# Kernel tuning notes

Measured on AMD Instinct MI355X. Metric: run time of the kernel, lower is better.

## Reference

```python
import jax, jax.numpy as jnp
import numpy as np

N_NODES = 50000
N_EDGES = 1200000
IN_CH = 128
HID = 64
HEADS = 1
OUT_CH = 64
NEG_SLOPE = 0.2


def setup_inputs() -> dict:
    key = jax.random.key(0)
    ks = jax.random.split(key, 9)
    x = jax.random.normal(ks[0], (N_NODES, IN_CH), dtype=jnp.float32)
    edge_index = jax.random.randint(ks[1], (2, N_EDGES), 0, N_NODES, dtype=jnp.int64)
    edge_weight = jax.random.uniform(ks[2], (N_EDGES,), dtype=jnp.float32)
    # GATv2Conv params: separate lin_l / lin_r (share_weights=False), attention vector, bias
    s_in = 1.0 / np.sqrt(IN_CH)
    W_l = jax.random.uniform(ks[3], (HEADS * HID, IN_CH), minval=-s_in, maxval=s_in, dtype=jnp.float32)
    W_r = jax.random.uniform(ks[4], (HEADS * HID, IN_CH), minval=-s_in, maxval=s_in, dtype=jnp.float32)
    att = jax.random.normal(ks[5], (HEADS, HID), dtype=jnp.float32) * (1.0 / np.sqrt(HID))
    bias_conv = jnp.zeros((HEADS * HID,), dtype=jnp.float32)
    s_h = 1.0 / np.sqrt(HEADS * HID)
    W_lin = jax.random.uniform(ks[6], (OUT_CH, HEADS * HID), minval=-s_h, maxval=s_h, dtype=jnp.float32)
    b_lin = jax.random.uniform(ks[7], (OUT_CH,), minval=-s_h, maxval=s_h, dtype=jnp.float32)
    return {"x": x, "edge_index": edge_index, "edge_weight": edge_weight,
            "W_l": W_l, "W_r": W_r, "att": att, "bias_conv": bias_conv,
            "W_lin": W_lin, "b_lin": b_lin}


def reference(x, edge_index, edge_weight, W_l, W_r, att, bias_conv, W_lin, b_lin):
    N = x.shape[0]
    H, C = att.shape
    # add self loops (GATv2Conv default add_self_loops=True)
    loop = jnp.arange(N, dtype=edge_index.dtype)
    src = jnp.concatenate([edge_index[0], loop])  # [E+N] source j
    dst = jnp.concatenate([edge_index[1], loop])  # [E+N] target i
    # linear projections -> [N, H, C]
    xl = (x @ W_l.T).reshape(N, H, C)
    xr = (x @ W_r.T).reshape(N, H, C)
    # per-edge GATv2 logits: att . LeakyReLU(xl_j + xr_i)
    e = jax.nn.leaky_relu(xl[src] + xr[dst], NEG_SLOPE)       # [E, H, C]
    logits = jnp.einsum('ehc,hc->eh', e, att)                 # [E, H]
    # segment softmax over incoming edges of each target node
    m = jax.ops.segment_max(logits, dst, num_segments=N)       # [N, H]
    m = jnp.where(jnp.isfinite(m), m, 0.0)
    expv = jnp.exp(logits - m[dst])                            # [E, H]
    denom = jax.ops.segment_sum(expv, dst, num_segments=N)     # [N, H]
    alpha = expv / (denom[dst] + 1e-16)                        # [E, H]
    # dropout(p=0.2) on alpha: identity in eval mode
    # scatter-weighted aggregation of source features
    msg = alpha[:, :, None] * xl[src]                          # [E, H, C]
    out = jax.ops.segment_sum(msg, dst, num_segments=N)        # [N, H, C]
    out = out.reshape(N, H * C) + bias_conv
    out = jax.nn.elu(out)
    return out @ W_lin.T + b_lin
```

## Files before the change

kernel.cpp:

```cpp
#include <hip/hip_runtime.h>

#define IN_CH 128
#define HID 64
#define NEG 0.2f

typedef short bf16x8 __attribute__((ext_vector_type(8)));
typedef float f32x4  __attribute__((ext_vector_type(4)));

__device__ __forceinline__ unsigned short f2bf(float f) {
    unsigned u = __float_as_uint(f);
    u += 0x7fffu + ((u >> 16) & 1u);
    return (unsigned short)(u >> 16);
}
__device__ __forceinline__ float bf2f(unsigned short h) {
    return __uint_as_float((unsigned)h << 16);
}

__global__ __launch_bounds__(512, 4) void proj_kernel(
    const float* __restrict__ x, const float* __restrict__ W_l,
    const float* __restrict__ W_r,
    unsigned short* __restrict__ xlb, float* __restrict__ xr,
    const int* __restrict__ dst, int* __restrict__ bcnt,
    int nN, int E)
{
    __shared__ unsigned short A_hi[64 * 136];
    __shared__ unsigned short A_lo[64 * 136];
    int tid = threadIdx.x;
    int nb = blockIdx.x * 64;
    int lane = tid & 63;
    int wid = __builtin_amdgcn_readfirstlane(tid >> 6);
    int mat = wid >> 2;
    int ct  = (wid & 3) * 16;
    int n = lane & 15, quad = lane >> 4;

    const float* __restrict__ W = mat ? W_r : W_l;
    bf16x8 Bh[4], Bl[4];
    #pragma unroll
    for (int s = 0; s < 4; ++s) {
        const float* wr = W + (size_t)(ct + n) * IN_CH + s * 32 + quad * 8;
        float4 w0 = *(const float4*)(wr);
        float4 w1 = *(const float4*)(wr + 4);
        float wf[8] = {w0.x, w0.y, w0.z, w0.w, w1.x, w1.y, w1.z, w1.w};
        #pragma unroll
        for (int j = 0; j < 8; ++j) {
            unsigned short h = f2bf(wf[j]);
            Bh[s][j] = (short)h;
            Bl[s][j] = (short)f2bf(wf[j] - bf2f(h));
        }
    }

    #pragma unroll
    for (int it = 0; it < 2; ++it) {
        int gi = it * 512 + tid;
        int row = gi >> 4, c8 = gi & 15;
        int node = nb + row;
        uint4 hi = make_uint4(0, 0, 0, 0), lo = make_uint4(0, 0, 0, 0);
        if (node < nN) {
            const float* xp = x + (size_t)node * IN_CH + c8 * 8;
            float4 f0 = *(const float4*)(xp);
            float4 f1 = *(const float4*)(xp + 4);
            float xf[8] = {f0.x, f0.y, f0.z, f0.w, f1.x, f1.y, f1.z, f1.w};
            unsigned hh[8], ll[8];
            #pragma unroll
            for (int j = 0; j < 8; ++j) {
                unsigned short h = f2bf(xf[j]);
                hh[j] = h;
                ll[j] = f2bf(xf[j] - bf2f(h));
            }
            hi = make_uint4(hh[0] | (hh[1] << 16), hh[2] | (hh[3] << 16),
                            hh[4] | (hh[5] << 16), hh[6] | (hh[7] << 16));
            lo = make_uint4(ll[0] | (ll[1] << 16), ll[2] | (ll[3] << 16),
                            ll[4] | (ll[5] << 16), ll[6] | (ll[7] << 16));
        }
        *(uint4*)(&A_hi[row * 136 + c8 * 8]) = hi;
        *(uint4*)(&A_lo[row * 136 + c8 * 8]) = lo;
    }
    __syncthreads();

    #pragma unroll
    for (int mt = 0; mt < 4; ++mt) {
        f32x4 d = {0.f, 0.f, 0.f, 0.f};
        int arow = (mt * 16 + n) * 136 + quad * 8;
        #pragma unroll
        for (int s = 0; s < 4; ++s) {
            bf16x8 ah = *(const bf16x8*)(&A_hi[arow + s * 32]);
            bf16x8 al = *(const bf16x8*)(&A_lo[arow + s * 32]);
            d = __builtin_amdgcn_mfma_f32_16x16x32_bf16(ah, Bh[s], d, 0, 0, 0);
            d = __builtin_amdgcn_mfma_f32_16x16x32_bf16(ah, Bl[s], d, 0, 0, 0);
            d = __builtin_amdgcn_mfma_f32_16x16x32_bf16(al, Bh[s], d, 0, 0, 0);
        }
        #pragma unroll
        for (int r = 0; r < 4; ++r) {
            int node = nb + mt * 16 + quad * 4 + r;
            if (node < nN) {
                if (mat)
                    xr[(size_t)node * HID + ct + n] = d[r];
                else
                    xlb[(size_t)node * HID + ct + n] = f2bf(d[r]);
            }
        }
    }

    __syncthreads();
    int* lh = (int*)A_hi;
    #pragma unroll
    for (int i = 0; i < 2; ++i) lh[i * 512 + tid] = 0;
    __syncthreads();
    int E4 = E >> 2;
    int gstride = gridDim.x * 512;
    for (int i = blockIdx.x * 512 + tid; i < E4; i += gstride) {
        int4 v = *(const int4*)(dst + i * 4);
        atomicAdd(&lh[v.x >> 6], 1);
        atomicAdd(&lh[v.y >> 6], 1);
        atomicAdd(&lh[v.z >> 6], 1);
        atomicAdd(&lh[v.w >> 6], 1);
    }
    if (blockIdx.x == 0 && tid == 0) {
        for (int i = E4 * 4; i < E; ++i) atomicAdd(&bcnt[dst[i] >> 6], 1);
    }
    __syncthreads();
    #pragma unroll
    for (int i = 0; i < 2; ++i) {
        int b = i * 512 + tid;
        int c = lh[b];
        if (c) atomicAdd(&bcnt[b], c);
    }
}

__global__ __launch_bounds__(256) void bscan_kernel(
    const int* __restrict__ bcnt, int* __restrict__ bstart,
    int* __restrict__ gcursor)
{
    __shared__ int wsum[4];
    int tid = threadIdx.x, lane = tid & 63, w = tid >> 6;
    int4 v = ((const int4*)bcnt)[tid];
    int e1 = v.x, e2 = v.x + v.y, e3 = e2 + v.z;
    int run = e3 + v.w;
    int sv = run;
    #pragma unroll
    for (int d = 1; d < 64; d <<= 1) {
        int t = __shfl_up(sv, d, 64);
        if (lane >= d) sv += t;
    }
    if (lane == 63) wsum[w] = sv;
    __syncthreads();
    if (tid < 4) {
        int t = wsum[tid];
        #pragma unroll
        for (int d = 1; d < 4; d <<= 1) {
            int u = __shfl_up(t, d, 64);
            if (tid >= d) t += u;
        }
        wsum[tid] = t;
    }
    __syncthreads();
    int off = (w ? wsum[w - 1] : 0) + (sv - run);
    int4 o = make_int4(off, off + e1, off + e2, off + e3);
    ((int4*)(bstart))[tid] = o;
    ((int4*)(gcursor))[tid] = o;
}

__global__ __launch_bounds__(256) void part_kernel(
    const int* __restrict__ src, const int* __restrict__ dst,
    int* __restrict__ gcursor, unsigned* __restrict__ pairs, int E)
{
    __shared__ int lhist[1024];
    __shared__ int lbase[1024];
    __shared__ int lcnt[1024];
    int tid = threadIdx.x;
    #pragma unroll
    for (int i = 0; i < 4; ++i) {
        lhist[i * 256 + tid] = 0;
        lcnt[i * 256 + tid] = 0;
    }
    __syncthreads();
    int base = blockIdx.x * 8192 + tid * 32;
    unsigned wreg[32];
    unsigned short bk[32];
    int v = E - base;
    v = v < 0 ? 0 : (v > 32 ? 32 : v);
    #pragma unroll
    for (int q = 0; q < 8; ++q) {
        int i = base + q * 4;
        if (i + 3 < E) {
            int4 s4 = *(const int4*)(src + i);
            int4 d4 = *(const int4*)(dst + i);
            wreg[q*4+0] = (unsigned)s4.x | (((unsigned)d4.x & 63u) << 16); bk[q*4+0] = d4.x >> 6;
            wreg[q*4+1] = (unsigned)s4.y | (((unsigned)d4.y & 63u) << 16); bk[q*4+1] = d4.y >> 6;
            wreg[q*4+2] = (unsigned)s4.z | (((unsigned)d4.z & 63u) << 16); bk[q*4+2] = d4.z >> 6;
            wreg[q*4+3] = (unsigned)s4.w | (((unsigned)d4.w & 63u) << 16); bk[q*4+3] = d4.w >> 6;
        } else {
            for (int j = 0; j < 4; ++j) {
                int e = i + j;
                if (e < E) {
                    int s = src[e], d = dst[e];
                    wreg[q*4+j] = (unsigned)s | (((unsigned)d & 63u) << 16);
                    bk[q*4+j] = d >> 6;
                }
            }
        }
    }
    for (int q = 0; q < v; ++q) atomicAdd(&lhist[bk[q]], 1);
    __syncthreads();
    #pragma unroll
    for (int i = 0; i < 4; ++i) {
        int b = i * 256 + tid;
        int c = lhist[b];
        lbase[b] = c ? atomicAdd(&gcursor[b], c) : 0;
    }
    __syncthreads();
    for (int q = 0; q < v; ++q) {
        int b = bk[q];
        int r = atomicAdd(&lcnt[b], 1);
        pairs[lbase[b] + r] = wreg[q];
    }
}

__global__ __launch_bounds__(256, 8) void gat_sorted(
    const unsigned short* __restrict__ xlb, const float* __restrict__ xr,
    const unsigned* __restrict__ pairs, const int* __restrict__ bstart,
    const float* __restrict__ att, const float* __restrict__ bias_conv,
    const float* __restrict__ W_lin, const float* __restrict__ b_lin,
    float* __restrict__ out, int nN)
{
    __shared__ unsigned short sorted[2048];
    __shared__ unsigned short Hhi[32 * 72];
    __shared__ unsigned short Hlo[32 * 72];
    __shared__ int cnt[32];
    __shared__ int rs[33];
    __shared__ int cur[32];
    int tid = threadIdx.x;
    if (tid < 32) cnt[tid] = 0;
    __syncthreads();

    int blk = blockIdx.x;
    int b  = blk >> 1;
    int hh = blk & 1;
    int e0 = bstart[b];
    int M = bstart[b + 1] - e0;
    if (M > 2048) M = 2048;

    unsigned ew[8];
    int ne = 0;
    for (int i = tid; i < M; i += 256) {
        unsigned w = pairs[e0 + i];
        int d6 = (w >> 16) & 63;
        if ((d6 >> 5) == hh) {
            ew[ne++] = w;
            atomicAdd(&cnt[d6 & 31], 1);
        }
    }
    __syncthreads();
    if (tid < 32) {
        int c = cnt[tid];
        int s = c;
        #pragma unroll
        for (int d = 1; d < 32; d <<= 1) {
            int t = __shfl_up(s, d, 64);
            if (tid >= d) s += t;
        }
        rs[tid] = s - c;
        cur[tid] = s - c;
        if (tid == 31) rs[32] = s;
    }
    __syncthreads();
    for (int q = 0; q < ne; ++q) {
        unsigned w = ew[q];
        int d = (w >> 16) & 31;
        int p = atomicAdd(&cur[d], 1);
        sorted[p] = (unsigned short)(w & 0xFFFFu);
    }
    __syncthreads();

    int lane = tid & 63, wv = tid >> 6;
    int g = lane >> 4, gl = lane & 15;
    const float4 att4 = *(const float4*)(att + gl * 4);
    int nb = b * 64 + hh * 32;
    for (int t = 0; t < 8; ++t) {
        int nl = wv * 8 + t;
        int node = nb + nl;
        if (node >= nN) break;
        const float4 xr4 = *(const float4*)(xr + (size_t)node * HID + gl * 4);
        float4 acc = make_float4(0.f, 0.f, 0.f, 0.f);
        float denom = 0.f;
        if (g == 0) {
            ushort4 us = *(const ushort4*)(xlb + (size_t)node * HID + gl * 4);
            float xsx = bf2f(us.x), xsy = bf2f(us.y), xsz = bf2f(us.z), xsw = bf2f(us.w);
            float tx = xsx + xr4.x, ty = xsy + xr4.y;
            float tz = xsz + xr4.z, tw = xsw + xr4.w;
            float r =          att4.x * (fmaxf(tx, 0.f) + NEG * fminf(tx, 0.f));
            r = fmaf(att4.y, fmaxf(ty, 0.f) + NEG * fminf(ty, 0.f), r);
            r = fmaf(att4.z, fmaxf(tz, 0.f) + NEG * fminf(tz, 0.f), r);
            r = fmaf(att4.w, fmaxf(tw, 0.f) + NEG * fminf(tw, 0.f), r);
            r += __shfl_xor(r, 1, 64);
            r += __shfl_xor(r, 2, 64);
            r += __shfl_xor(r, 4, 64);
            r += __shfl_xor(r, 8, 64);
            float ev = __expf(r);
            denom = ev;
            acc.x = ev * xsx; acc.y = ev * xsy;
            acc.z = ev * xsz; acc.w = ev * xsw;
        }
        int s0 = rs[nl], s1 = rs[nl + 1];
        int last = s1 - 1;
        for (int base = s0; base < s1; base += 16) {
            int kb = base + g * 4;
            int k0 = (kb     <= last) ? kb     : last;
            int k1 = (kb + 1 <= last) ? kb + 1 : last;
            int k2 = (kb + 2 <= last) ? kb + 2 : last;
            int k3 = (kb + 3 <= last) ? kb + 3 : last;
            int j0 = sorted[k0], j1 = sorted[k1], j2 = sorted[k2], j3 = sorted[k3];
            ushort4 ua = *(const ushort4*)(xlb + (size_t)j0 * HID + gl * 4);
            ushort4 ub = *(const ushort4*)(xlb + (size_t)j1 * HID + gl * 4);
            ushort4 uc = *(const ushort4*)(xlb + (size_t)j2 * HID + gl * 4);
            ushort4 ud = *(const ushort4*)(xlb + (size_t)j3 * HID + gl * 4);
            float xax = bf2f(ua.x), xay = bf2f(ua.y), xaz = bf2f(ua.z), xaw = bf2f(ua.w);
            float xbx = bf2f(ub.x), xby = bf2f(ub.y), xbz = bf2f(ub.z), xbw = bf2f(ub.w);
            float xcx = bf2f(uc.x), xcy = bf2f(uc.y), xcz = bf2f(uc.z), xcw = bf2f(uc.w);
            float xdx = bf2f(ud.x), xdy = bf2f(ud.y), xdz = bf2f(ud.z), xdw = bf2f(ud.w);

            float t0, t1, t2, t3, ra, rb, rc, rd;
            t0 = xax + xr4.x; t1 = xay + xr4.y; t2 = xaz + xr4.z; t3 = xaw + xr4.w;
            ra =          att4.x * (fmaxf(t0, 0.f) + NEG * fminf(t0, 0.f));
            ra = fmaf(att4.y, fmaxf(t1, 0.f) + NEG * fminf(t1, 0.f), ra);
            ra = fmaf(att4.z, fmaxf(t2, 0.f) + NEG * fminf(t2, 0.f), ra);
            ra = fmaf(att4.w, fmaxf(t3, 0.f) + NEG * fminf(t3, 0.f), ra);
            t0 = xbx + xr4.x; t1 = xby + xr4.y; t2 = xbz + xr4.z; t3 = xbw + xr4.w;
            rb =          att4.x * (fmaxf(t0, 0.f) + NEG * fminf(t0, 0.f));
            rb = fmaf(att4.y, fmaxf(t1, 0.f) + NEG * fminf(t1, 0.f), rb);
            rb = fmaf(att4.z, fmaxf(t2, 0.f) + NEG * fminf(t2, 0.f), rb);
            rb = fmaf(att4.w, fmaxf(t3, 0.f) + NEG * fminf(t3, 0.f), rb);
            t0 = xcx + xr4.x; t1 = xcy + xr4.y; t2 = xcz + xr4.z; t3 = xcw + xr4.w;
            rc =          att4.x * (fmaxf(t0, 0.f) + NEG * fminf(t0, 0.f));
            rc = fmaf(att4.y, fmaxf(t1, 0.f) + NEG * fminf(t1, 0.f), rc);
            rc = fmaf(att4.z, fmaxf(t2, 0.f) + NEG * fminf(t2, 0.f), rc);
            rc = fmaf(att4.w, fmaxf(t3, 0.f) + NEG * fminf(t3, 0.f), rc);
            t0 = xdx + xr4.x; t1 = xdy + xr4.y; t2 = xdz + xr4.z; t3 = xdw + xr4.w;
            rd =          att4.x * (fmaxf(t0, 0.f) + NEG * fminf(t0, 0.f));
            rd = fmaf(att4.y, fmaxf(t1, 0.f) + NEG * fminf(t1, 0.f), rd);
            rd = fmaf(att4.z, fmaxf(t2, 0.f) + NEG * fminf(t2, 0.f), rd);
            rd = fmaf(att4.w, fmaxf(t3, 0.f) + NEG * fminf(t3, 0.f), rd);

            ra += __shfl_xor(ra, 1, 64); rb += __shfl_xor(rb, 1, 64);
            rc += __shfl_xor(rc, 1, 64); rd += __shfl_xor(rd, 1, 64);
            ra += __shfl_xor(ra, 2, 64); rb += __shfl_xor(rb, 2, 64);
            rc += __shfl_xor(rc, 2, 64); rd += __shfl_xor(rd, 2, 64);
            ra += __shfl_xor(ra, 4, 64); rb += __shfl_xor(rb, 4, 64);
            rc += __shfl_xor(rc, 4, 64); rd += __shfl_xor(rd, 4, 64);
            ra += __shfl_xor(ra, 8, 64); rb += __shfl_xor(rb, 8, 64);
            rc += __shfl_xor(rc, 8, 64); rd += __shfl_xor(rd, 8, 64);

            float ea = (kb     < s1) ? __expf(ra) : 0.f;
            float eb = (kb + 1 < s1) ? __expf(rb) : 0.f;
            float ec = (kb + 2 < s1) ? __expf(rc) : 0.f;
            float ed = (kb + 3 < s1) ? __expf(rd) : 0.f;
            denom += (ea + eb) + (ec + ed);
            acc.x = fmaf(ea, xax, acc.x); acc.x = fmaf(eb, xbx, acc.x);
            acc.x = fmaf(ec, xcx, acc.x); acc.x = fmaf(ed, xdx, acc.x);
            acc.y = fmaf(ea, xay, acc.y); acc.y = fmaf(eb, xby, acc.y);
            acc.y = fmaf(ec, xcy, acc.y); acc.y = fmaf(ed, xdy, acc.y);
            acc.z = fmaf(ea, xaz, acc.z); acc.z = fmaf(eb, xbz, acc.z);
            acc.z = fmaf(ec, xcz, acc.z); acc.z = fmaf(ed, xdz, acc.z);
            acc.w = fmaf(ea, xaw, acc.w); acc.w = fmaf(eb, xbw, acc.w);
            acc.w = fmaf(ec, xcw, acc.w); acc.w = fmaf(ed, xdw, acc.w);
        }
        denom += __shfl_xor(denom, 16, 64);
        denom += __shfl_xor(denom, 32, 64);
        acc.x += __shfl_xor(acc.x, 16, 64); acc.x += __shfl_xor(acc.x, 32, 64);
        acc.y += __shfl_xor(acc.y, 16, 64); acc.y += __shfl_xor(acc.y, 32, 64);
        acc.z += __shfl_xor(acc.z, 16, 64); acc.z += __shfl_xor(acc.z, 32, 64);
        acc.w += __shfl_xor(acc.w, 16, 64); acc.w += __shfl_xor(acc.w, 32, 64);
        float inv = 1.f / (denom + 1e-16f);
        float4 b4 = *(const float4*)(bias_conv + gl * 4);
        float hx = fmaf(acc.x, inv, b4.x);
        float hy = fmaf(acc.y, inv, b4.y);
        float hz = fmaf(acc.z, inv, b4.z);
        float hw = fmaf(acc.w, inv, b4.w);
        hx = (hx > 0.f) ? hx : (__expf(hx) - 1.f);
        hy = (hy > 0.f) ? hy : (__expf(hy) - 1.f);
        hz = (hz > 0.f) ? hz : (__expf(hz) - 1.f);
        hw = (hw > 0.f) ? hw : (__expf(hw) - 1.f);
        if (g == 0) {
            unsigned short hix = f2bf(hx), hiy = f2bf(hy),
                           hiz = f2bf(hz), hiw = f2bf(hw);
            ushort4 vhi = make_ushort4(hix, hiy, hiz, hiw);
            ushort4 vlo = make_ushort4(f2bf(hx - bf2f(hix)), f2bf(hy - bf2f(hiy)),
                                       f2bf(hz - bf2f(hiz)), f2bf(hw - bf2f(hiw)));
            *(ushort4*)(&Hhi[nl * 72 + gl * 4]) = vhi;
            *(ushort4*)(&Hlo[nl * 72 + gl * 4]) = vlo;
        }
    }
    __syncthreads();

    bf16x8 Wh[2], Wl[2];
    #pragma unroll
    for (int s = 0; s < 2; ++s) {
        const float* wr = W_lin + (size_t)(wv * 16 + gl) * HID + s * 32 + g * 8;
        float4 w0 = *(const float4*)(wr);
        float4 w1 = *(const float4*)(wr + 4);
        float wf[8] = {w0.x, w0.y, w0.z, w0.w, w1.x, w1.y, w1.z, w1.w};
        #pragma unroll
        for (int j = 0; j < 8; ++j) {
            unsigned short h = f2bf(wf[j]);
            Wh[s][j] = (short)h;
            Wl[s][j] = (short)f2bf(wf[j] - bf2f(h));
        }
    }
    float blin = b_lin[wv * 16 + gl];
    #pragma unroll
    for (int mt = 0; mt < 2; ++mt) {
        f32x4 d = {0.f, 0.f, 0.f, 0.f};
        int arow = (mt * 16 + gl) * 72 + g * 8;
        #pragma unroll
        for (int s = 0; s < 2; ++s) {
            bf16x8 ah = *(const bf16x8*)(&Hhi[arow + s * 32]);
            bf16x8 al = *(const bf16x8*)(&Hlo[arow + s * 32]);
            d = __builtin_amdgcn_mfma_f32_16x16x32_bf16(ah, Wh[s], d, 0, 0, 0);
            d = __builtin_amdgcn_mfma_f32_16x16x32_bf16(ah, Wl[s], d, 0, 0, 0);
            d = __builtin_amdgcn_mfma_f32_16x16x32_bf16(al, Wh[s], d, 0, 0, 0);
        }
        #pragma unroll
        for (int r = 0; r < 4; ++r) {
            int node = nb + mt * 16 + g * 4 + r;
            if (node < nN)
                out[(size_t)node * HID + wv * 16 + gl] = d[r] + blin;
        }
    }
}

extern "C" void kernel_launch(void* const* d_in, const int* in_sizes, int n_in,
                              void* d_out, int out_size, void* d_ws, size_t ws_size,
                              hipStream_t stream) {
    const float* x      = (const float*)d_in[0];
    const int*   ei     = (const int*)d_in[1];
    const float* W_l    = (const float*)d_in[3];
    const float* W_r    = (const float*)d_in[4];
    const float* att    = (const float*)d_in[5];
    const float* bias_c = (const float*)d_in[6];
    const float* W_lin  = (const float*)d_in[7];
    const float* b_lin  = (const float*)d_in[8];
    float* out = (float*)d_out;

    int N = in_sizes[0] / IN_CH;
    int E = in_sizes[2];
    const int* srcp = ei;
    const int* dstp = ei + E;
    int NB = (N + 63) / 64;

    char* ws = (char*)d_ws;
    float* xr = (float*)ws;
    unsigned short* xlb = (unsigned short*)(xr + (size_t)N * HID);
    int* bcnt    = (int*)(xlb + (size_t)N * HID);
    int* bstart  = bcnt + 1024;
    int* gcursor = bstart + 1056;
    unsigned* pairs = (unsigned*)(gcursor + 1024);

    hipMemsetAsync(bcnt, 0, 1024 * sizeof(int), stream);
    proj_kernel<<<NB, 512, 0, stream>>>(x, W_l, W_r, xlb, xr, dstp, bcnt, N, E);
    bscan_kernel<<<1, 256, 0, stream>>>(bcnt, bstart, gcursor);
    part_kernel<<<(E + 8191) / 8192, 256, 0, stream>>>(srcp, dstp, gcursor, pairs, E);
    gat_sorted<<<NB * 2, 256, 0, stream>>>(xlb, xr, pairs, bstart,
                                           att, bias_c, W_lin, b_lin, out, N);
}
```

Measured before the change: 200.9 us.

## Merge histogram, scan, and partition into one grid-synced prep kernel

Moves the destination-bucket histogram out of the projection kernel and combines histogram, prefix scan and partition into one persistent kernel. The stages are separated by software grid barriers on atomic counters. Block 0 of the projection kernel now zeroes the counters in place of a separate memset, which removes two launches. The LeakyReLU attention dot is also rewritten as a*t + b*|t| with pre-scaled att vectors, which cuts ALU ops per edge. The spin barriers depend on all 512 blocks being co-resident, and the partition pass now reads src/dst twice.

```diff
diff --git a/kernel.cpp b/kernel.cpp
--- a/kernel.cpp
+++ b/kernel.cpp
@@ -20,8 +20,8 @@
     const float* __restrict__ x, const float* __restrict__ W_l,
     const float* __restrict__ W_r,
     unsigned short* __restrict__ xlb, float* __restrict__ xr,
-    const int* __restrict__ dst, int* __restrict__ bcnt,
-    int nN, int E)
+    int* __restrict__ zbuf,
+    int nN)
 {
     __shared__ unsigned short A_hi[64 * 136];
     __shared__ unsigned short A_lo[64 * 136];
@@ -32,6 +32,10 @@
     int mat = wid >> 2;
     int ct  = (wid & 3) * 16;
     int n = lane & 15, quad = lane >> 4;
+
+    if (blockIdx.x == 0) {
+        for (int i = tid; i < 1056; i += 512) zbuf[i] = 0;
+    }
 
     const float* __restrict__ W = mat ? W_r : W_l;
     bf16x8 Bh[4], Bl[4];
@@ -100,108 +104,95 @@
             }
         }
     }
-
-    __syncthreads();
-    int* lh = (int*)A_hi;
-    #pragma unroll
-    for (int i = 0; i < 2; ++i) lh[i * 512 + tid] = 0;
-    __syncthreads();
-    int E4 = E >> 2;
-    int gstride = gridDim.x * 512;
-    for (int i = blockIdx.x * 512 + tid; i < E4; i += gstride) {
-        int4 v = *(const int4*)(dst + i * 4);
-        atomicAdd(&lh[v.x >> 6], 1);
-        atomicAdd(&lh[v.y >> 6], 1);
-        atomicAdd(&lh[v.z >> 6], 1);
-        atomicAdd(&lh[v.w >> 6], 1);
-    }
-    if (blockIdx.x == 0 && tid == 0) {
-        for (int i = E4 * 4; i < E; ++i) atomicAdd(&bcnt[dst[i] >> 6], 1);
-    }
-    __syncthreads();
-    #pragma unroll
-    for (int i = 0; i < 2; ++i) {
-        int b = i * 512 + tid;
-        int c = lh[b];
-        if (c) atomicAdd(&bcnt[b], c);
-    }
-}
-
-__global__ __launch_bounds__(256) void bscan_kernel(
-    const int* __restrict__ bcnt, int* __restrict__ bstart,
-    int* __restrict__ gcursor)
-{
-    __shared__ int wsum[4];
-    int tid = threadIdx.x, lane = tid & 63, w = tid >> 6;
-    int4 v = ((const int4*)bcnt)[tid];
-    int e1 = v.x, e2 = v.x + v.y, e3 = e2 + v.z;
-    int run = e3 + v.w;
-    int sv = run;
-    #pragma unroll
-    for (int d = 1; d < 64; d <<= 1) {
-        int t = __shfl_up(sv, d, 64);
-        if (lane >= d) sv += t;
-    }
-    if (lane == 63) wsum[w] = sv;
-    __syncthreads();
-    if (tid < 4) {
-        int t = wsum[tid];
-        #pragma unroll
-        for (int d = 1; d < 4; d <<= 1) {
-            int u = __shfl_up(t, d, 64);
-            if (tid >= d) t += u;
-        }
-        wsum[tid] = t;
-    }
-    __syncthreads();
-    int off = (w ? wsum[w - 1] : 0) + (sv - run);
-    int4 o = make_int4(off, off + e1, off + e2, off + e3);
-    ((int4*)(bstart))[tid] = o;
-    ((int4*)(gcursor))[tid] = o;
-}
-
-__global__ __launch_bounds__(256) void part_kernel(
+}
+
+__device__ __forceinline__ void grid_sync_dev(int* counter, int target) {
+    __syncthreads();
+    if (threadIdx.x == 0) {
+        __threadfence();
+        atomicAdd(counter, 1);
+        while (__hip_atomic_load(counter, __ATOMIC_RELAXED,
+                                 __HIP_MEMORY_SCOPE_AGENT) < target)
+            __builtin_amdgcn_s_sleep(2);
+        __threadfence();
+    }
+    __syncthreads();
+}
+
+__global__ __launch_bounds__(256, 4) void prep_kernel(
     const int* __restrict__ src, const int* __restrict__ dst,
-    int* __restrict__ gcursor, unsigned* __restrict__ pairs, int E)
+    int* __restrict__ bcnt, int* __restrict__ bstart,
+    int* __restrict__ gcursor, int* __restrict__ bars,
+    unsigned* __restrict__ pairs, int E)
 {
     __shared__ int lhist[1024];
     __shared__ int lbase[1024];
     __shared__ int lcnt[1024];
-    int tid = threadIdx.x;
+    __shared__ int wsum[4];
+    int tid = threadIdx.x, bid = blockIdx.x, G = gridDim.x;
     #pragma unroll
     for (int i = 0; i < 4; ++i) {
         lhist[i * 256 + tid] = 0;
         lcnt[i * 256 + tid] = 0;
     }
     __syncthreads();
-    int base = blockIdx.x * 8192 + tid * 32;
-    unsigned wreg[32];
-    unsigned short bk[32];
-    int v = E - base;
-    v = v < 0 ? 0 : (v > 32 ? 32 : v);
-    #pragma unroll
-    for (int q = 0; q < 8; ++q) {
-        int i = base + q * 4;
-        if (i + 3 < E) {
-            int4 s4 = *(const int4*)(src + i);
+
+    int C = ((E + G - 1) / G + 3) & ~3;
+    int lo = bid * C;
+    int hi = lo + C; if (hi > E) hi = E;
+
+    for (int i = lo + tid * 4; i < hi; i += 1024) {
+        if (i + 3 < hi) {
             int4 d4 = *(const int4*)(dst + i);
-            wreg[q*4+0] = (unsigned)s4.x | (((unsigned)d4.x & 63u) << 16); bk[q*4+0] = d4.x >> 6;
-            wreg[q*4+1] = (unsigned)s4.y | (((unsigned)d4.y & 63u) << 16); bk[q*4+1] = d4.y >> 6;
-            wreg[q*4+2] = (unsigned)s4.z | (((unsigned)d4.z & 63u) << 16); bk[q*4+2] = d4.z >> 6;
-            wreg[q*4+3] = (unsigned)s4.w | (((unsigned)d4.w & 63u) << 16); bk[q*4+3] = d4.w >> 6;
+            atomicAdd(&lhist[d4.x >> 6], 1);
+            atomicAdd(&lhist[d4.y >> 6], 1);
+            atomicAdd(&lhist[d4.z >> 6], 1);
+            atomicAdd(&lhist[d4.w >> 6], 1);
         } else {
-            for (int j = 0; j < 4; ++j) {
-                int e = i + j;
-                if (e < E) {
-                    int s = src[e], d = dst[e];
-                    wreg[q*4+j] = (unsigned)s | (((unsigned)d & 63u) << 16);
-                    bk[q*4+j] = d >> 6;
-                }
+            for (int j = i; j < hi; ++j) atomicAdd(&lhist[dst[j] >> 6], 1);
+        }
+    }
+    __syncthreads();
+    #pragma unroll
+    for (int i = 0; i < 4; ++i) {
+        int b = i * 256 + tid;
+        int c = lhist[b];
+        if (c) atomicAdd(&bcnt[b], c);
+    }
+
+    grid_sync_dev(&bars[0], G);
+
+    if (bid == 0) {
+        int lane = tid & 63, w = tid >> 6;
+        int4 v = ((const int4*)bcnt)[tid];
+        int e1 = v.x, e2 = v.x + v.y, e3 = e2 + v.z;
+        int run = e3 + v.w;
+        int sv = run;
+        #pragma unroll
+        for (int d = 1; d < 64; d <<= 1) {
+            int t = __shfl_up(sv, d, 64);
+            if (lane >= d) sv += t;
+        }
+        if (lane == 63) wsum[w] = sv;
+        __syncthreads();
+        if (tid < 4) {
+            int t = wsum[tid];
+            #pragma unroll
+            for (int d = 1; d < 4; d <<= 1) {
+                int u = __shfl_up(t, d, 64);
+                if (tid >= d) t += u;
             }
-        }
-    }
-    for (int q = 0; q < v; ++q) atomicAdd(&lhist[bk[q]], 1);
-    __syncthreads();
+            wsum[tid] = t;
+        }
+        __syncthreads();
+        int off = (w ? wsum[w - 1] : 0) + (sv - run);
+        int4 o = make_int4(off, off + e1, off + e2, off + e3);
+        ((int4*)(bstart))[tid] = o;
+        ((int4*)(gcursor))[tid] = o;
+    }
+
+    grid_sync_dev(&bars[1], G);
+
     #pragma unroll
     for (int i = 0; i < 4; ++i) {
         int b = i * 256 + tid;
@@ -209,10 +200,25 @@
         lbase[b] = c ? atomicAdd(&gcursor[b], c) : 0;
     }
     __syncthreads();
-    for (int q = 0; q < v; ++q) {
-        int b = bk[q];
-        int r = atomicAdd(&lcnt[b], 1);
-        pairs[lbase[b] + r] = wreg[q];
+    for (int i = lo + tid * 4; i < hi; i += 1024) {
+        if (i + 3 < hi) {
+            int4 s4 = *(const int4*)(src + i);
+            int4 d4 = *(const int4*)(dst + i);
+            { int b = d4.x >> 6; int r = atomicAdd(&lcnt[b], 1);
+              pairs[lbase[b] + r] = (unsigned)s4.x | (((unsigned)d4.x & 63u) << 16); }
+            { int b = d4.y >> 6; int r = atomicAdd(&lcnt[b], 1);
+              pairs[lbase[b] + r] = (unsigned)s4.y | (((unsigned)d4.y & 63u) << 16); }
+            { int b = d4.z >> 6; int r = atomicAdd(&lcnt[b], 1);
+              pairs[lbase[b] + r] = (unsigned)s4.z | (((unsigned)d4.z & 63u) << 16); }
+            { int b = d4.w >> 6; int r = atomicAdd(&lcnt[b], 1);
+              pairs[lbase[b] + r] = (unsigned)s4.w | (((unsigned)d4.w & 63u) << 16); }
+        } else {
+            for (int j = i; j < hi; ++j) {
+                int s = src[j], d = dst[j];
+                int b = d >> 6; int r = atomicAdd(&lcnt[b], 1);
+                pairs[lbase[b] + r] = (unsigned)s | (((unsigned)d & 63u) << 16);
+            }
+        }
     }
 }
 
@@ -275,6 +281,9 @@
     int lane = tid & 63, wv = tid >> 6;
     int g = lane >> 4, gl = lane & 15;
     const float4 att4 = *(const float4*)(att + gl * 4);
+    const float c1 = 0.5f * (1.f + NEG), c2 = 0.5f * (1.f - NEG);
+    float4 a1 = make_float4(c1 * att4.x, c1 * att4.y, c1 * att4.z, c1 * att4.w);
+    float4 a2 = make_float4(c2 * att4.x, c2 * att4.y, c2 * att4.z, c2 * att4.w);
     int nb = b * 64 + hh * 32;
     for (int t = 0; t < 8; ++t) {
         int nl = wv * 8 + t;
@@ -288,10 +297,11 @@
             float xsx = bf2f(us.x), xsy = bf2f(us.y), xsz = bf2f(us.z), xsw = bf2f(us.w);
             float tx = xsx + xr4.x, ty = xsy + xr4.y;
             float tz = xsz + xr4.z, tw = xsw + xr4.w;
-            float r =          att4.x * (fmaxf(tx, 0.f) + NEG * fminf(tx, 0.f));
-            r = fmaf(att4.y, fmaxf(ty, 0.f) + NEG * fminf(ty, 0.f), r);
-            r = fmaf(att4.z, fmaxf(tz, 0.f) + NEG * fminf(tz, 0.f), r);
-            r = fmaf(att4.w, fmaxf(tw, 0.f) + NEG * fminf(tw, 0.f), r);
+            float r = a1.x * tx;
+            r = fmaf(a2.x, fabsf(tx), r);
+            r = fmaf(a1.y, ty, r); r = fmaf(a2.y, fabsf(ty), r);
+            r = fmaf(a1.z, tz, r); r = fmaf(a2.z, fabsf(tz), r);
+            r = fmaf(a1.w, tw, r); r = fmaf(a2.w, fabsf(tw), r);
             r += __shfl_xor(r, 1, 64);
             r += __shfl_xor(r, 2, 64);
             r += __shfl_xor(r, 4, 64);
@@ -321,25 +331,25 @@
 
             float t0, t1, t2, t3, ra, rb, rc, rd;
             t0 = xax + xr4.x; t1 = xay + xr4.y; t2 = xaz + xr4.z; t3 = xaw + xr4.w;
-            ra =          att4.x * (fmaxf(t0, 0.f) + NEG * fminf(t0, 0.f));
-            ra = fmaf(att4.y, fmaxf(t1, 0.f) + NEG * fminf(t1, 0.f), ra);
-            ra = fmaf(att4.z, fmaxf(t2, 0.f) + NEG * fminf(t2, 0.f), ra);
-            ra = fmaf(att4.w, fmaxf(t3, 0.f) + NEG * fminf(t3, 0.f), ra);
+            ra = a1.x * t0;        ra = fmaf(a2.x, fabsf(t0), ra);
+            ra = fmaf(a1.y, t1, ra); ra = fmaf(a2.y, fabsf(t1), ra);
+            ra = fmaf(a1.z, t2, ra); ra = fmaf(a2.z, fabsf(t2), ra);
+            ra = fmaf(a1.w, t3, ra); ra = fmaf(a2.w, fabsf(t3), ra);
             t0 = xbx + xr4.x; t1 = xby + xr4.y; t2 = xbz + xr4.z; t3 = xbw + xr4.w;
-            rb =          att4.x * (fmaxf(t0, 0.f) + NEG * fminf(t0, 0.f));
-            rb = fmaf(att4.y, fmaxf(t1, 0.f) + NEG * fminf(t1, 0.f), rb);
-            rb = fmaf(att4.z, fmaxf(t2, 0.f) + NEG * fminf(t2, 0.f), rb);
-            rb = fmaf(att4.w, fmaxf(t3, 0.f) + NEG * fminf(t3, 0.f), rb);
+            rb = a1.x * t0;        rb = fmaf(a2.x, fabsf(t0), rb);
+            rb = fmaf(a1.y, t1, rb); rb = fmaf(a2.y, fabsf(t1), rb);
+            rb = fmaf(a1.z, t2, rb); rb = fmaf(a2.z, fabsf(t2), rb);
+            rb = fmaf(a1.w, t3, rb); rb = fmaf(a2.w, fabsf(t3), rb);
             t0 = xcx + xr4.x; t1 = xcy + xr4.y; t2 = xcz + xr4.z; t3 = xcw + xr4.w;
-            rc =          att4.x * (fmaxf(t0, 0.f) + NEG * fminf(t0, 0.f));
-            rc = fmaf(att4.y, fmaxf(t1, 0.f) + NEG * fminf(t1, 0.f), rc);
-            rc = fmaf(att4.z, fmaxf(t2, 0.f) + NEG * fminf(t2, 0.f), rc);
-            rc = fmaf(att4.w, fmaxf(t3, 0.f) + NEG * fminf(t3, 0.f), rc);
+            rc = a1.x * t0;        rc = fmaf(a2.x, fabsf(t0), rc);
+            rc = fmaf(a1.y, t1, rc); rc = fmaf(a2.y, fabsf(t1), rc);
+            rc = fmaf(a1.z, t2, rc); rc = fmaf(a2.z, fabsf(t2), rc);
+            rc = fmaf(a1.w, t3, rc); rc = fmaf(a2.w, fabsf(t3), rc);
             t0 = xdx + xr4.x; t1 = xdy + xr4.y; t2 = xdz + xr4.z; t3 = xdw + xr4.w;
-            rd =          att4.x * (fmaxf(t0, 0.f) + NEG * fminf(t0, 0.f));
-            rd = fmaf(att4.y, fmaxf(t1, 0.f) + NEG * fminf(t1, 0.f), rd);
-            rd = fmaf(att4.z, fmaxf(t2, 0.f) + NEG * fminf(t2, 0.f), rd);
-            rd = fmaf(att4.w, fmaxf(t3, 0.f) + NEG * fminf(t3, 0.f), rd);
+            rd = a1.x * t0;        rd = fmaf(a2.x, fabsf(t0), rd);
+            rd = fmaf(a1.y, t1, rd); rd = fmaf(a2.y, fabsf(t1), rd);
+            rd = fmaf(a1.z, t2, rd); rd = fmaf(a2.z, fabsf(t2), rd);
+            rd = fmaf(a1.w, t3, rd); rd = fmaf(a2.w, fabsf(t3), rd);
 
             ra += __shfl_xor(ra, 1, 64); rb += __shfl_xor(rb, 1, 64);
             rc += __shfl_xor(rc, 1, 64); rd += __shfl_xor(rd, 1, 64);
@@ -451,14 +461,18 @@
     float* xr = (float*)ws;
     unsigned short* xlb = (unsigned short*)(xr + (size_t)N * HID);
     int* bcnt    = (int*)(xlb + (size_t)N * HID);
-    int* bstart  = bcnt + 1024;
+    int* bars    = bcnt + 1024;
+    int* bstart  = bars + 32;
     int* gcursor = bstart + 1056;
     unsigned* pairs = (unsigned*)(gcursor + 1024);
 
-    hipMemsetAsync(bcnt, 0, 1024 * sizeof(int), stream);
-    proj_kernel<<<NB, 512, 0, stream>>>(x, W_l, W_r, xlb, xr, dstp, bcnt, N, E);
-    bscan_kernel<<<1, 256, 0, stream>>>(bcnt, bstart, gcursor);
-    part_kernel<<<(E + 8191) / 8192, 256, 0, stream>>>(srcp, dstp, gcursor, pairs, E);
+    int PG = (E + 2047) / 2048;
+    if (PG > 512) PG = 512;
+    if (PG < 1) PG = 1;
+
+    proj_kernel<<<NB, 512, 0, stream>>>(x, W_l, W_r, xlb, xr, bcnt, N);
+    prep_kernel<<<PG, 256, 0, stream>>>(srcp, dstp, bcnt, bstart, gcursor,
+                                        bars, pairs, E);
     gat_sorted<<<NB * 2, 256, 0, stream>>>(xlb, xr, pairs, bstart,
                                            att, bias_c, W_lin, b_lin, out, N);
 }
```

Measured after the change: 258.7 us. 1.29x slower.
